# Performance work log

Measured on AMD Instinct MI355X. Metric: run time of the kernel, lower is better.

The kernel has to match this reference:

```python
import jax, jax.numpy as jnp
import numpy as np

B, A, S, NC = 32, 3, 80, 80
EPS = 1e-7
LS = 0.1  # label smoothing


def setup_inputs() -> dict:
    key = jax.random.key(0)
    k1, k2, k3, k4, k5, k6 = jax.random.split(key, 6)
    pred = jax.random.normal(k1, (B, A, S, S, 5 + NC), dtype=jnp.float32)
    # structured target: obj flag in {0,1}, box cxcywh, class id (as float)
    obj = (jax.random.uniform(k2, (B, A, S, S)) < 0.05).astype(jnp.float32)
    xy = jax.random.uniform(k3, (B, A, S, S, 2))
    wh = jax.random.uniform(k4, (B, A, S, S, 2), minval=0.5, maxval=4.0)
    cls = jax.random.randint(k5, (B, A, S, S), 0, NC).astype(jnp.float32)
    target = jnp.concatenate([obj[..., None], xy, wh, cls[..., None]], axis=-1)
    anchors = jax.random.uniform(k6, (A, 2), minval=1.0, maxval=4.0)
    return {"pred": pred, "target": target, "anchors": anchors}


def _bce_logits(z, t):
    # numerically-stable BCEWithLogits: max(z,0) - z*t + log(1+exp(-|z|))
    return jnp.maximum(z, 0.0) - z * t + jnp.log1p(jnp.exp(-jnp.abs(z)))


def _masked_mean(x, m):
    return jnp.sum(x * m) / jnp.maximum(jnp.sum(m), 1.0)


def _ciou(b1, b2):
    # boxes [..., 4] in (cx, cy, w, h)
    cx1, cy1, w1, h1 = b1[..., 0], b1[..., 1], b1[..., 2], b1[..., 3]
    cx2, cy2, w2, h2 = b2[..., 0], b2[..., 1], b2[..., 2], b2[..., 3]
    x1a, x1b = cx1 - w1 * 0.5, cx1 + w1 * 0.5
    y1a, y1b = cy1 - h1 * 0.5, cy1 + h1 * 0.5
    x2a, x2b = cx2 - w2 * 0.5, cx2 + w2 * 0.5
    y2a, y2b = cy2 - h2 * 0.5, cy2 + h2 * 0.5
    iw = jnp.clip(jnp.minimum(x1b, x2b) - jnp.maximum(x1a, x2a), 0.0)
    ih = jnp.clip(jnp.minimum(y1b, y2b) - jnp.maximum(y1a, y2a), 0.0)
    inter = iw * ih
    union = w1 * h1 + w2 * h2 - inter + EPS
    iou = inter / union
    cw = jnp.maximum(x1b, x2b) - jnp.minimum(x1a, x2a)  # enclosing box
    ch = jnp.maximum(y1b, y2b) - jnp.minimum(y1a, y2a)
    c2 = cw * cw + ch * ch + EPS
    rho2 = (cx2 - cx1) ** 2 + (cy2 - cy1) ** 2
    four_over_pi2 = 4.0 / (np.pi ** 2)
    v = four_over_pi2 * (jnp.arctan(w2 / (h2 + EPS)) - jnp.arctan(w1 / (h1 + EPS))) ** 2
    alpha = v / (1.0 - iou + v + EPS)
    return iou - rho2 / c2 - alpha * v


def reference(pred, target, anchors):
    obj = (target[..., 0] == 1.0).astype(pred.dtype)    # [B,A,S,S]
    no_obj = (target[..., 0] == 0.0).astype(pred.dtype)
    # no-object BCE-with-logits on objectness channel (masked mean)
    no_object_loss = _masked_mean(_bce_logits(pred[..., 0], target[..., 0]), no_obj)
    # decoded box predictions: sigmoid xy, exp(wh)*anchors
    anc = anchors.reshape(1, A, 1, 1, 2)
    box_preds = jnp.concatenate(
        [jax.nn.sigmoid(pred[..., 1:3]), jnp.exp(pred[..., 3:5]) * anc], axis=-1)
    cious = _ciou(box_preds, target[..., 1:5])          # [B,A,S,S]
    box_loss = _masked_mean(1.0 - cious, obj)
    # note: original passes sigmoid(pred) INTO BCEWithLogits -> keep that quirk
    object_loss = _masked_mean(_bce_logits(jax.nn.sigmoid(pred[..., 0]), target[..., 0]), obj)
    # label-smoothed cross entropy on class logits
    logp = jax.nn.log_softmax(pred[..., 5:], axis=-1)   # [B,A,S,S,NC]
    cls_idx = target[..., 5].astype(jnp.int32)
    logp_y = jnp.take_along_axis(logp, cls_idx[..., None], axis=-1)[..., 0]
    ce = -((1.0 - LS) * logp_y + (LS / NC) * jnp.sum(logp, axis=-1))
    class_loss = _masked_mean(ce, obj)
    return 2.0 * box_loss + object_loss + no_object_loss + class_loss
```

## Files before the change

### kernel.cpp

```cpp
#include <hip/hip_runtime.h>
#include <cmath>

constexpr int Bn = 32, An = 3, Sn = 80, NCc = 80;
constexpr int NCELL = Bn * An * Sn * Sn;
constexpr int BDIM  = 256;
constexpr int NBLK  = NCELL / BDIM;
constexpr float EPSc = 1e-7f;

__device__ __forceinline__ float bce_logits(float z, float t) {
    return fmaxf(z, 0.f) - z * t + log1pf(expf(-fabsf(z)));
}

__global__ __launch_bounds__(BDIM) void yolo_main(
    const float* __restrict__ pred, const float* __restrict__ target,
    const float* __restrict__ anchors, float* __restrict__ partials)
{
    const int i    = blockIdx.x * BDIM + threadIdx.x;
    const int lane = threadIdx.x & 63;

    const float* tt = target + (size_t)i * 6;
    const float* pp = pred   + (size_t)i * 85;

    const float t0 = tt[0];
    const float z0 = pp[0];
    const bool obj   = (t0 == 1.0f);
    const bool noobj = (t0 == 0.0f);

    float nsum = 0.f, ncnt = 0.f, bsum = 0.f, osum = 0.f, csum = 0.f, ocnt = 0.f;

    if (noobj) {
        nsum = bce_logits(z0, t0);
        ncnt = 1.f;
    }

    if (obj) {
        const float p1 = pp[1], p2 = pp[2], p3 = pp[3], p4 = pp[4];
        const float px = 1.f / (1.f + expf(-p1));
        const float py = 1.f / (1.f + expf(-p2));
        const int   a  = (i / (Sn * Sn)) % An;
        const float pw = expf(p3) * anchors[2 * a];
        const float ph = expf(p4) * anchors[2 * a + 1];
        const float tx = tt[1], ty = tt[2], tw = tt[3], th = tt[4];

        const float x1a = px - pw * 0.5f, x1b = px + pw * 0.5f;
        const float y1a = py - ph * 0.5f, y1b = py + ph * 0.5f;
        const float x2a = tx - tw * 0.5f, x2b = tx + tw * 0.5f;
        const float y2a = ty - th * 0.5f, y2b = ty + th * 0.5f;

        const float iw = fmaxf(fminf(x1b, x2b) - fmaxf(x1a, x2a), 0.f);
        const float ih = fmaxf(fminf(y1b, y2b) - fmaxf(y1a, y2a), 0.f);
        const float inter = iw * ih;
        const float uni   = pw * ph + tw * th - inter + EPSc;
        const float iou   = inter / uni;

        const float cw = fmaxf(x1b, x2b) - fminf(x1a, x2a);
        const float ch = fmaxf(y1b, y2b) - fminf(y1a, y2a);
        const float c2 = cw * cw + ch * ch + EPSc;
        const float rho2 = (tx - px) * (tx - px) + (ty - py) * (ty - py);

        const float fopi2 = 4.0f / (3.14159265358979323846f * 3.14159265358979323846f);
        const float dv = atanf(tw / (th + EPSc)) - atanf(pw / (ph + EPSc));
        const float v  = fopi2 * dv * dv;
        const float alpha = v / (1.f - iou + v + EPSc);
        const float ciou  = iou - rho2 / c2 - alpha * v;

        bsum = 1.f - ciou;

        const float s0 = 1.f / (1.f + expf(-z0));
        osum = bce_logits(s0, t0);
        ocnt = 1.f;
    }

    unsigned long long mask = __ballot(obj);
    const int wave_base = i - lane;
    while (mask) {
        const int lj = __builtin_ctzll(mask);
        mask &= mask - 1;
        const int cj = wave_base + lj;

        const float* pc = pred + (size_t)cj * 85 + 5;
        const float z1 = pc[lane];
        const float z2 = (lane < NCc - 64) ? pc[64 + lane] : -INFINITY;

        float m = fmaxf(z1, z2);
        #pragma unroll
        for (int off = 32; off; off >>= 1) m = fmaxf(m, __shfl_xor(m, off));

        float e  = expf(z1 - m) + ((lane < NCc - 64) ? expf(z2 - m) : 0.f);
        float sz = z1 + ((lane < NCc - 64) ? z2 : 0.f);
        #pragma unroll
        for (int off = 32; off; off >>= 1) {
            e  += __shfl_xor(e, off);
            sz += __shfl_xor(sz, off);
        }
        const float lse = m + logf(e);

        const int k = (int)target[(size_t)cj * 6 + 5];
        const float zk = (k < 64) ? __shfl(z1, k) : __shfl(z2, k - 64);

        const float logp_y   = zk - lse;
        const float sum_logp = sz - (float)NCc * lse;
        const float ce = -(0.9f * logp_y + (0.1f / (float)NCc) * sum_logp);
        if (lane == 0) csum += ce;
    }

    #pragma unroll
    for (int off = 32; off; off >>= 1) {
        nsum += __shfl_xor(nsum, off);
        ncnt += __shfl_xor(ncnt, off);
        bsum += __shfl_xor(bsum, off);
        osum += __shfl_xor(osum, off);
        csum += __shfl_xor(csum, off);
        ocnt += __shfl_xor(ocnt, off);
    }

    __shared__ float red[4][6];
    const int w = threadIdx.x >> 6;
    if (lane == 0) {
        red[w][0] = nsum; red[w][1] = ncnt; red[w][2] = bsum;
        red[w][3] = osum; red[w][4] = csum; red[w][5] = ocnt;
    }
    __syncthreads();
    if (threadIdx.x < 6) {
        const int j = threadIdx.x;
        partials[(size_t)blockIdx.x * 8 + j] =
            red[0][j] + red[1][j] + red[2][j] + red[3][j];
    }
}

__global__ __launch_bounds__(256) void yolo_reduce(
    const float* __restrict__ partials, float* __restrict__ out)
{
    float s[6] = {0.f, 0.f, 0.f, 0.f, 0.f, 0.f};
    for (int b = threadIdx.x; b < NBLK; b += 256) {
        #pragma unroll
        for (int j = 0; j < 6; ++j) s[j] += partials[(size_t)b * 8 + j];
    }
    #pragma unroll
    for (int off = 32; off; off >>= 1) {
        #pragma unroll
        for (int j = 0; j < 6; ++j) s[j] += __shfl_xor(s[j], off);
    }
    __shared__ float red[4][6];
    const int w = threadIdx.x >> 6, lane = threadIdx.x & 63;
    if (lane == 0) {
        #pragma unroll
        for (int j = 0; j < 6; ++j) red[w][j] = s[j];
    }
    __syncthreads();
    if (threadIdx.x == 0) {
        float n[6];
        #pragma unroll
        for (int j = 0; j < 6; ++j)
            n[j] = red[0][j] + red[1][j] + red[2][j] + red[3][j];
        const float noobj_l = n[0] / fmaxf(n[1], 1.f);
        const float box_l   = n[2] / fmaxf(n[5], 1.f);
        const float obj_l   = n[3] / fmaxf(n[5], 1.f);
        const float cls_l   = n[4] / fmaxf(n[5], 1.f);
        out[0] = 2.f * box_l + obj_l + noobj_l + cls_l;
    }
}

extern "C" void kernel_launch(void* const* d_in, const int* in_sizes, int n_in,
                              void* d_out, int out_size, void* d_ws, size_t ws_size,
                              hipStream_t stream) {
    const float* pred    = (const float*)d_in[0];
    const float* target  = (const float*)d_in[1];
    const float* anchors = (const float*)d_in[2];
    float* out = (float*)d_out;
    float* partials = (float*)d_ws;

    yolo_main<<<NBLK, BDIM, 0, stream>>>(pred, target, anchors, partials);
    yolo_reduce<<<1, 256, 0, stream>>>(partials, out);
}
```

Measured before the change: 284.2 us.

## Compact object cells into a global list and process them in a separate kernel

Splits the fused kernel into passes. The first pass computes the objectness terms for every cell and compacts object-cell indices into a global list with a block-level atomic. A second grid of fixed size then evaluates CIoU per thread and the class cross-entropy per wave over that list, accumulating with float atomics. The aim is to remove the per-wave serial loop over object cells and its load imbalance. In exchange it adds two kernel launches, a global index buffer with an indirect gather, a fixed cap on the list size, and order-dependent float atomics.

```diff
diff --git a/kernel.cpp b/kernel.cpp
--- a/kernel.cpp
+++ b/kernel.cpp
@@ -4,40 +4,92 @@
 constexpr int Bn = 32, An = 3, Sn = 80, NCc = 80;
 constexpr int NCELL = Bn * An * Sn * Sn;
 constexpr int BDIM  = 256;
-constexpr int NBLK  = NCELL / BDIM;
+constexpr int NBLK1 = NCELL / BDIM;
+constexpr int NBLK2 = 512;
+constexpr int LIST_CAP = 131072;
 constexpr float EPSc = 1e-7f;
 
-__device__ __forceinline__ float bce_logits(float z, float t) {
-    return fmaxf(z, 0.f) - z * t + log1pf(expf(-fabsf(z)));
-}
-
-__global__ __launch_bounds__(BDIM) void yolo_main(
+
+__global__ __launch_bounds__(64) void yolo_init(int* ws_i) {
+    if (threadIdx.x < 16) ws_i[threadIdx.x] = 0;
+}
+
+__global__ __launch_bounds__(BDIM) void yolo_k1(
     const float* __restrict__ pred, const float* __restrict__ target,
-    const float* __restrict__ anchors, float* __restrict__ partials)
+    int* __restrict__ cnt, int* __restrict__ list, float* __restrict__ partials)
 {
     const int i    = blockIdx.x * BDIM + threadIdx.x;
     const int lane = threadIdx.x & 63;
-
-    const float* tt = target + (size_t)i * 6;
-    const float* pp = pred   + (size_t)i * 85;
-
-    const float t0 = tt[0];
-    const float z0 = pp[0];
-    const bool obj   = (t0 == 1.0f);
-    const bool noobj = (t0 == 0.0f);
-
-    float nsum = 0.f, ncnt = 0.f, bsum = 0.f, osum = 0.f, csum = 0.f, ocnt = 0.f;
-
-    if (noobj) {
-        nsum = bce_logits(z0, t0);
-        ncnt = 1.f;
-    }
-
+    const int wv   = threadIdx.x >> 6;
+
+    const float t0 = target[(size_t)i * 6];
+    const float z0 = pred[(size_t)i * 85];
+    const bool obj = (t0 == 1.0f);
+
+    float nsum = 0.f, osum = 0.f;
+    if (t0 == 0.0f) {
+        nsum = fmaxf(z0, 0.f) + log1pf(expf(-fabsf(z0)));
+    }
     if (obj) {
+        const float s = 1.f / (1.f + expf(-z0));
+        osum = log1pf(expf(-s));
+    }
+
+    const unsigned long long b = __ballot(obj);
+    __shared__ int wcnt[4];
+    __shared__ int wbase[4];
+    if (lane == 0) wcnt[wv] = __popcll(b);
+    __syncthreads();
+    if (threadIdx.x == 0) {
+        const int tot = wcnt[0] + wcnt[1] + wcnt[2] + wcnt[3];
+        const int base = tot ? atomicAdd(cnt, tot) : 0;
+        wbase[0] = base;
+        wbase[1] = base + wcnt[0];
+        wbase[2] = base + wcnt[0] + wcnt[1];
+        wbase[3] = base + wcnt[0] + wcnt[1] + wcnt[2];
+    }
+    __syncthreads();
+    if (obj) {
+        const int pos = wbase[wv] + __popcll(b & ((1ull << lane) - 1ull));
+        if (pos < LIST_CAP) list[pos] = i;
+    }
+
+    #pragma unroll
+    for (int off = 32; off; off >>= 1) {
+        nsum += __shfl_xor(nsum, off);
+        osum += __shfl_xor(osum, off);
+    }
+    __shared__ float red[4][2];
+    if (lane == 0) { red[wv][0] = nsum; red[wv][1] = osum; }
+    __syncthreads();
+    if (threadIdx.x < 2) {
+        const int j = threadIdx.x;
+        partials[(size_t)blockIdx.x * 2 + j] =
+            red[0][j] + red[1][j] + red[2][j] + red[3][j];
+    }
+}
+
+__global__ __launch_bounds__(BDIM) void yolo_k2(
+    const float* __restrict__ pred, const float* __restrict__ target,
+    const float* __restrict__ anchors,
+    const int* __restrict__ cnt, const int* __restrict__ list,
+    float* __restrict__ acc)
+{
+    const int M = min(*cnt, LIST_CAP);
+    const int lane = threadIdx.x & 63;
+    const int wv   = threadIdx.x >> 6;
+    const int tid  = blockIdx.x * BDIM + threadIdx.x;
+
+    float bsum = 0.f;
+    for (int t = tid; t < M; t += NBLK2 * BDIM) {
+        const int ci = list[t];
+        const float* pp = pred   + (size_t)ci * 85;
+        const float* tt = target + (size_t)ci * 6;
+
         const float p1 = pp[1], p2 = pp[2], p3 = pp[3], p4 = pp[4];
         const float px = 1.f / (1.f + expf(-p1));
         const float py = 1.f / (1.f + expf(-p2));
-        const int   a  = (i / (Sn * Sn)) % An;
+        const int   a  = (ci / (Sn * Sn)) % An;
         const float pw = expf(p3) * anchors[2 * a];
         const float ph = expf(p4) * anchors[2 * a + 1];
         const float tx = tt[1], ty = tt[2], tw = tt[3], th = tt[4];
@@ -63,22 +115,15 @@
         const float v  = fopi2 * dv * dv;
         const float alpha = v / (1.f - iou + v + EPSc);
         const float ciou  = iou - rho2 / c2 - alpha * v;
-
-        bsum = 1.f - ciou;
-
-        const float s0 = 1.f / (1.f + expf(-z0));
-        osum = bce_logits(s0, t0);
-        ocnt = 1.f;
-    }
-
-    unsigned long long mask = __ballot(obj);
-    const int wave_base = i - lane;
-    while (mask) {
-        const int lj = __builtin_ctzll(mask);
-        mask &= mask - 1;
-        const int cj = wave_base + lj;
-
-        const float* pc = pred + (size_t)cj * 85 + 5;
+        bsum += 1.f - ciou;
+    }
+
+    float csum = 0.f;
+    const int wglob = tid >> 6;
+    const int nwaves = NBLK2 * (BDIM / 64);
+    for (int c = wglob; c < M; c += nwaves) {
+        const int ci = list[c];
+        const float* pc = pred + (size_t)ci * 85 + 5;
         const float z1 = pc[lane];
         const float z2 = (lane < NCc - 64) ? pc[64 + lane] : -INFINITY;
 
@@ -95,7 +140,7 @@
         }
         const float lse = m + logf(e);
 
-        const int k = (int)target[(size_t)cj * 6 + 5];
+        const int k = (int)target[(size_t)ci * 6 + 5];
         const float zk = (k < 64) ? __shfl(z1, k) : __shfl(z2, k - 64);
 
         const float logp_y   = zk - lse;
@@ -106,57 +151,47 @@
 
     #pragma unroll
     for (int off = 32; off; off >>= 1) {
-        nsum += __shfl_xor(nsum, off);
-        ncnt += __shfl_xor(ncnt, off);
         bsum += __shfl_xor(bsum, off);
-        osum += __shfl_xor(osum, off);
         csum += __shfl_xor(csum, off);
-        ocnt += __shfl_xor(ocnt, off);
-    }
-
-    __shared__ float red[4][6];
-    const int w = threadIdx.x >> 6;
-    if (lane == 0) {
-        red[w][0] = nsum; red[w][1] = ncnt; red[w][2] = bsum;
-        red[w][3] = osum; red[w][4] = csum; red[w][5] = ocnt;
-    }
-    __syncthreads();
-    if (threadIdx.x < 6) {
-        const int j = threadIdx.x;
-        partials[(size_t)blockIdx.x * 8 + j] =
-            red[0][j] + red[1][j] + red[2][j] + red[3][j];
-    }
-}
-
-__global__ __launch_bounds__(256) void yolo_reduce(
-    const float* __restrict__ partials, float* __restrict__ out)
+    }
+    __shared__ float red[4][2];
+    if (lane == 0) { red[wv][0] = bsum; red[wv][1] = csum; }
+    __syncthreads();
+    if (threadIdx.x == 0) {
+        const float bs = red[0][0] + red[1][0] + red[2][0] + red[3][0];
+        const float cs = red[0][1] + red[1][1] + red[2][1] + red[3][1];
+        atomicAdd(&acc[0], bs);
+        atomicAdd(&acc[1], cs);
+    }
+}
+
+__global__ __launch_bounds__(256) void yolo_finish(
+    const float* __restrict__ partials, const int* __restrict__ cnt,
+    const float* __restrict__ acc, float* __restrict__ out)
 {
-    float s[6] = {0.f, 0.f, 0.f, 0.f, 0.f, 0.f};
-    for (int b = threadIdx.x; b < NBLK; b += 256) {
-        #pragma unroll
-        for (int j = 0; j < 6; ++j) s[j] += partials[(size_t)b * 8 + j];
+    float s0 = 0.f, s1 = 0.f;
+    for (int b = threadIdx.x; b < NBLK1; b += 256) {
+        s0 += partials[(size_t)b * 2];
+        s1 += partials[(size_t)b * 2 + 1];
     }
     #pragma unroll
     for (int off = 32; off; off >>= 1) {
-        #pragma unroll
-        for (int j = 0; j < 6; ++j) s[j] += __shfl_xor(s[j], off);
-    }
-    __shared__ float red[4][6];
-    const int w = threadIdx.x >> 6, lane = threadIdx.x & 63;
-    if (lane == 0) {
-        #pragma unroll
-        for (int j = 0; j < 6; ++j) red[w][j] = s[j];
-    }
+        s0 += __shfl_xor(s0, off);
+        s1 += __shfl_xor(s1, off);
+    }
+    __shared__ float red[4][2];
+    const int wv = threadIdx.x >> 6, lane = threadIdx.x & 63;
+    if (lane == 0) { red[wv][0] = s0; red[wv][1] = s1; }
     __syncthreads();
     if (threadIdx.x == 0) {
-        float n[6];
-        #pragma unroll
-        for (int j = 0; j < 6; ++j)
-            n[j] = red[0][j] + red[1][j] + red[2][j] + red[3][j];
-        const float noobj_l = n[0] / fmaxf(n[1], 1.f);
-        const float box_l   = n[2] / fmaxf(n[5], 1.f);
-        const float obj_l   = n[3] / fmaxf(n[5], 1.f);
-        const float cls_l   = n[4] / fmaxf(n[5], 1.f);
+        const float nsum = red[0][0] + red[1][0] + red[2][0] + red[3][0];
+        const float osum = red[0][1] + red[1][1] + red[2][1] + red[3][1];
+        const int   M    = min(*cnt, LIST_CAP);
+        const float fM   = fmaxf((float)M, 1.f);
+        const float noobj_l = nsum / fmaxf((float)(NCELL - M), 1.f);
+        const float obj_l   = osum / fM;
+        const float box_l   = acc[0] / fM;
+        const float cls_l   = acc[1] / fM;
         out[0] = 2.f * box_l + obj_l + noobj_l + cls_l;
     }
 }
@@ -168,8 +203,15 @@
     const float* target  = (const float*)d_in[1];
     const float* anchors = (const float*)d_in[2];
     float* out = (float*)d_out;
-    float* partials = (float*)d_ws;
-
-    yolo_main<<<NBLK, BDIM, 0, stream>>>(pred, target, anchors, partials);
-    yolo_reduce<<<1, 256, 0, stream>>>(partials, out);
-}
+
+    int*   ws_i     = (int*)d_ws;
+    int*   cnt      = ws_i;
+    float* acc      = (float*)d_ws + 4;
+    float* partials = (float*)d_ws + 16;
+    int*   list     = ws_i + 8192;
+
+    yolo_init<<<1, 64, 0, stream>>>(ws_i);
+    yolo_k1<<<NBLK1, BDIM, 0, stream>>>(pred, target, cnt, list, partials);
+    yolo_k2<<<NBLK2, BDIM, 0, stream>>>(pred, target, anchors, cnt, list, acc);
+    yolo_finish<<<1, 256, 0, stream>>>(partials, cnt, acc, out);
+}
```

New measurement: 313.3 us. +10.2%, slower.
